# Performance work log

Measured on AMD Instinct MI355X. Metric: run time of the kernel, lower is better.

The kernel has to match this reference:

```python
import jax, jax.numpy as jnp
import numpy as np

N_USERS = 100000
N_ITEMS = 50000
N = N_USERS + N_ITEMS          # total graph nodes (users + items)
E = 128                        # emb_size
NNZ = 4_800_000                # edges per sparse adjacency (avg degree 32)
B = 4096                       # lookup batch
NL = 3                         # n_layers


def setup_inputs() -> dict:
    key = jax.random.key(0)
    ks = jax.random.split(key, 12)
    user_emb = jax.random.normal(ks[0], (N_USERS, E), jnp.float32) * 0.05
    item_emb = jax.random.normal(ks[1], (N_ITEMS, E), jnp.float32) * 0.05
    # COO edge lists for low-pass and high-pass normalized adjacencies.
    adj_row = jax.random.randint(ks[2], (NNZ,), 0, N)
    adj_col = jax.random.randint(ks[3], (NNZ,), 0, N)
    adj_val = jax.random.uniform(ks[4], (NNZ,), jnp.float32) / 32.0  # ~normalized weights
    hp_row = jax.random.randint(ks[5], (NNZ,), 0, N)
    hp_col = jax.random.randint(ks[6], (NNZ,), 0, N)
    hp_val = jax.random.uniform(ks[7], (NNZ,), jnp.float32) / 32.0
    # per-layer Linear(2E -> E): weight stored as [in, out] so y = x @ W + b
    W = jax.random.normal(ks[8], (NL, 2 * E, E), jnp.float32) * (1.0 / np.sqrt(2 * E))
    b = jnp.zeros((NL, E), jnp.float32)
    users = jax.random.randint(ks[9], (B,), 0, N_USERS)
    items = jax.random.randint(ks[10], (B,), 0, N_ITEMS)
    return dict(user_emb=user_emb, item_emb=item_emb, adj_val=adj_val, hp_val=hp_val,
                W=W, b=b, adj_row=adj_row, adj_col=adj_col,
                hp_row=hp_row, hp_col=hp_col, users=users, items=items)


def spmm(row, col, val, x):
    # sparse [N,N] @ dense [N,E] via gather + segment-sum
    return jax.ops.segment_sum(val[:, None] * x[col], row, num_segments=N)


def reference(user_emb, item_emb, adj_val, hp_val, W, b,
              adj_row, adj_col, hp_row, hp_col, users, items):
    ego = jnp.concatenate([user_emb, item_emb], axis=0)  # [N, E]
    pos = ego
    dis = ego
    for k in range(NL):
        pos = spmm(adj_row, adj_col, adj_val, pos)       # low-pass propagation
        dis = spmm(hp_row, hp_col, hp_val, dis)          # high-pass propagation
        ego = jnp.concatenate([pos, dis], axis=1) @ W[k] + b[k]  # [N, E]
        pos = ego
        dis = ego
    user_out = ego[users]                 # ego[:N_USERS][users]
    item_out = ego[N_USERS + items]       # ego[N_USERS:][items]
    return (user_out, item_out)
```

## Files before the change

kernel.cpp:

```cpp
#include <hip/hip_runtime.h>

#define N_USERS 100000
#define N_ITEMS 50000
#define NTOT    150000
#define E       128
#define NNZ     4800000
#define BATCH   4096
#define TILE    16
#define BSH     10
#define BROWS   1024
#define NBK     147
#define SLOT    16

typedef int v4i __attribute__((ext_vector_type(4)));

__device__ __forceinline__ int   ldnt_i(const int* p)   { return __builtin_nontemporal_load(p); }
__device__ __forceinline__ float ldnt_f(const float* p) { return __builtin_nontemporal_load(p); }
__device__ __forceinline__ v4i   ld_v4(const void* p)   { return *(const v4i*)p; }

__global__ __launch_bounds__(1024) void bucket_count(const int* __restrict__ rowA,
                                                     const int* __restrict__ rowH,
                                                     int* __restrict__ cntA,
                                                     int* __restrict__ cntH) {
    __shared__ int c[2 * NBK];
    for (int i = threadIdx.x; i < 2 * NBK; i += 1024) c[i] = 0;
    __syncthreads();
    int i = blockIdx.x * 1024 + threadIdx.x;
    const int stride = gridDim.x * 1024;
    for (; i < NNZ; i += stride) {
        atomicAdd(&c[ldnt_i(rowA + i) >> BSH], 1);
        atomicAdd(&c[NBK + (ldnt_i(rowH + i) >> BSH)], 1);
    }
    __syncthreads();
    for (int j = threadIdx.x; j < 2 * NBK; j += 1024) {
        const int v = c[j];
        if (v) atomicAdd(j < NBK ? (cntA + j) : (cntH + (j - NBK)), v);
    }
}

__global__ __launch_bounds__(64) void bucket_scan(const int* __restrict__ cntA,
                                                  const int* __restrict__ cntH,
                                                  int* __restrict__ baseA, int* __restrict__ baseH,
                                                  int* __restrict__ gcurA, int* __restrict__ gcurH) {
    const int t = threadIdx.x;
    if (t == 0) {
        int run = 0;
        for (int j = 0; j < NBK; ++j) { baseA[j] = run; gcurA[j] = run; run += cntA[j]; }
        baseA[NBK] = run;
    } else if (t == 1) {
        int run = 0;
        for (int j = 0; j < NBK; ++j) { baseH[j] = run; gcurH[j] = run; run += cntH[j]; }
        baseH[NBK] = run;
    }
}

__global__ __launch_bounds__(1024) void wc_scatter(const int* __restrict__ rowA, const int* __restrict__ colA,
                                                   const float* __restrict__ valA,
                                                   const int* __restrict__ rowH, const int* __restrict__ colH,
                                                   const float* __restrict__ valH,
                                                   int* __restrict__ gcurA, int* __restrict__ gcurH,
                                                   int2* __restrict__ stA, int2* __restrict__ stH) {
    __shared__ int  lcnt[2 * NBK];
    __shared__ int2 lent[2 * NBK * SLOT];
    for (int i = threadIdx.x; i < 2 * NBK; i += 1024) lcnt[i] = 0;
    __syncthreads();
    const int stride = gridDim.x * 1024;
    const int rounds = (NNZ + stride - 1) / stride;
    for (int rd = 0; rd < rounds; ++rd) {
        const int i = rd * stride + blockIdx.x * 1024 + threadIdx.x;
        if (i < NNZ) {
            {
                const int r = ldnt_i(rowA + i), cc = ldnt_i(colA + i);
                const float v = ldnt_f(valA + i);
                const int b = r >> BSH;
                const int2 pk = make_int2(((r & (BROWS - 1)) << 18) | cc, __float_as_int(v));
                const int n = atomicAdd(&lcnt[b], 1);
                if (n < SLOT) lent[b * SLOT + n] = pk;
                else          stA[atomicAdd(&gcurA[b], 1)] = pk;
            }
            {
                const int r = ldnt_i(rowH + i), cc = ldnt_i(colH + i);
                const float v = ldnt_f(valH + i);
                const int b = r >> BSH;
                const int gb = NBK + b;
                const int2 pk = make_int2(((r & (BROWS - 1)) << 18) | cc, __float_as_int(v));
                const int n = atomicAdd(&lcnt[gb], 1);
                if (n < SLOT) lent[gb * SLOT + n] = pk;
                else          stH[atomicAdd(&gcurH[b], 1)] = pk;
            }
        }
        __syncthreads();
        const int thresh = (rd == rounds - 1) ? 1 : 8;
        for (int gb = threadIdx.x; gb < 2 * NBK; gb += 1024) {
            int n = lcnt[gb]; if (n > SLOT) n = SLOT;
            if (n >= thresh) {
                int*  gc = (gb < NBK) ? &gcurA[gb] : &gcurH[gb - NBK];
                int2* st = (gb < NBK) ? stA : stH;
                const int p = atomicAdd(gc, n);
                for (int j = 0; j < n; ++j) st[p + j] = lent[gb * SLOT + j];
                lcnt[gb] = 0;
            }
        }
        __syncthreads();
    }
}

__global__ __launch_bounds__(1024) void bucket_csr(const int2* __restrict__ stA, const int2* __restrict__ stH,
                                                   const int* __restrict__ baseA, const int* __restrict__ baseH,
                                                   int* __restrict__ rpA, int* __restrict__ rpH,
                                                   int2* __restrict__ edA, int2* __restrict__ edH) {
    const int isH = blockIdx.x >= NBK;
    const int b   = isH ? blockIdx.x - NBK : blockIdx.x;
    const int2* st   = isH ? stH   : stA;
    const int*  base = isH ? baseH : baseA;
    int*  rp = isH ? rpH : rpA;
    int2* ed = isH ? edH : edA;
    const int s = base[b], e = base[b + 1];
    const int t = threadIdx.x, lane = t & 63, wv = t >> 6;
    __shared__ int cnt[BROWS];
    __shared__ int wsum[16], woff[16];
    cnt[t] = 0;
    __syncthreads();
    for (int i = s + t; i < e; i += 1024) atomicAdd(&cnt[st[i].x >> 18], 1);
    __syncthreads();
    const int v = cnt[t];
    int x = v;
    #pragma unroll
    for (int off = 1; off < 64; off <<= 1) {
        const int n = __shfl_up(x, off);
        if (lane >= off) x += n;
    }
    if (lane == 63) wsum[wv] = x;
    __syncthreads();
    if (t == 0) { int acc = 0; for (int w = 0; w < 16; ++w) { woff[w] = acc; acc += wsum[w]; } }
    __syncthreads();
    const int excl = woff[wv] + (x - v);
    const int rglob = (b << BSH) + t;
    if (rglob < NTOT) rp[rglob] = s + excl;
    __syncthreads();
    cnt[t] = excl;
    __syncthreads();
    for (int i = s + t; i < e; i += 1024) {
        const int2 pk = st[i];
        const int rl = pk.x >> 18;
        const int p = s + atomicAdd(&cnt[rl], 1);
        ed[p] = make_int2(pk.x & 0x3FFFF, pk.y);
    }
    if (t == 0 && b == 0) rp[NTOT] = NNZ;
}

__global__ __launch_bounds__(256) void copy_int(const int* __restrict__ src,
                                                int* __restrict__ dst, int n) {
    const int i = blockIdx.x * blockDim.x + threadIdx.x;
    if (i < n) dst[i] = src[i];
}

template<bool FIRST>
__device__ __forceinline__ const float4* rowbase(int c, const float* __restrict__ ue,
                                                 const float* __restrict__ ie,
                                                 const float* __restrict__ A) {
    if constexpr (FIRST)
        return (c < N_USERS) ? ((const float4*)ue + (size_t)c * (E / 4))
                             : ((const float4*)ie + (size_t)(c - N_USERS) * (E / 4));
    else
        return (const float4*)A + (size_t)c * (E / 4);
}

template<bool FIRST>
__device__ __forceinline__ void pairfma(v4i q, const float* __restrict__ ue,
                                        const float* __restrict__ ie,
                                        const float* __restrict__ A,
                                        int sub, int half, float4& acc) {
    const int   c = half ? q[2] : q[0];
    const float v = __int_as_float(half ? q[3] : q[1]);
    const float4 xv = rowbase<FIRST>(c, ue, ie, A)[sub];
    acc.x = fmaf(v, xv.x, acc.x);
    acc.y = fmaf(v, xv.y, acc.y);
    acc.z = fmaf(v, xv.z, acc.z);
    acc.w = fmaf(v, xv.w, acc.w);
}

template<bool FIRST>
__device__ __forceinline__ float4 row_accum(const int* __restrict__ rp,
                                            const int2* __restrict__ ed,
                                            const float* __restrict__ ue,
                                            const float* __restrict__ ie,
                                            const float* __restrict__ A,
                                            int r, int sub, int half) {
    const int s = rp[r];
    const int e = rp[r + 1];
    float4 accA = {0.f, 0.f, 0.f, 0.f};
    float4 accB = {0.f, 0.f, 0.f, 0.f};
    int i = s;
    if (i < e && (i & 1)) {
        const int2 t0 = ed[i];
        const float v = half ? 0.f : __int_as_float(t0.y);
        const float4 xv = rowbase<FIRST>(t0.x, ue, ie, A)[sub];
        accA.x = fmaf(v, xv.x, accA.x); accA.y = fmaf(v, xv.y, accA.y);
        accA.z = fmaf(v, xv.z, accA.z); accA.w = fmaf(v, xv.w, accA.w);
        ++i;
    }
    for (; i + 7 < e; i += 8) {
        const v4i q0 = ld_v4(ed + i);
        const v4i q1 = ld_v4(ed + i + 2);
        const v4i q2 = ld_v4(ed + i + 4);
        const v4i q3 = ld_v4(ed + i + 6);
        pairfma<FIRST>(q0, ue, ie, A, sub, half, accA);
        pairfma<FIRST>(q1, ue, ie, A, sub, half, accB);
        pairfma<FIRST>(q2, ue, ie, A, sub, half, accA);
        pairfma<FIRST>(q3, ue, ie, A, sub, half, accB);
    }
    for (; i + 1 < e; i += 2) {
        const v4i q = ld_v4(ed + i);
        pairfma<FIRST>(q, ue, ie, A, sub, half, accA);
    }
    if (i < e) {
        const int2 t0 = ed[i];
        const float v = half ? 0.f : __int_as_float(t0.y);
        const float4 xv = rowbase<FIRST>(t0.x, ue, ie, A)[sub];
        accA.x = fmaf(v, xv.x, accA.x); accA.y = fmaf(v, xv.y, accA.y);
        accA.z = fmaf(v, xv.z, accA.z); accA.w = fmaf(v, xv.w, accA.w);
    }
    return make_float4(accA.x + accB.x, accA.y + accB.y,
                       accA.z + accB.z, accA.w + accB.w);
}

template<bool FIRST, bool FINAL>
__global__ __launch_bounds__(256) void fused_layer(
    const float* __restrict__ A,
    const float* __restrict__ ue, const float* __restrict__ ie,
    const int* __restrict__ rpA, const int2* __restrict__ edA,
    const int* __restrict__ rpH, const int2* __restrict__ edH,
    const float* __restrict__ Wk, const float* __restrict__ bk,
    const int* __restrict__ users, const int* __restrict__ items,
    float* __restrict__ out) {
    __shared__ float sP[TILE][E];
    __shared__ float sD[TILE][E];
    const int t    = threadIdx.x;
    const int lane = t & 63;
    const int sub  = lane & 31;
    const int half = lane >> 5;
    const int wv   = t >> 6;
    const int r0   = blockIdx.x * TILE;

    for (int rl = wv * 4; rl < wv * 4 + 4; ++rl) {
        const int slot = r0 + rl;
        int r = slot;
        if constexpr (FINAL)
            r = (slot < BATCH) ? users[slot] : (N_USERS + items[slot - BATCH]);
        const float4 ap = row_accum<FIRST>(rpA, edA, ue, ie, A, r, sub, half);
        const float4 ad = row_accum<FIRST>(rpH, edH, ue, ie, A, r, sub, half);
        float4 send = half ? ap : ad;
        float4 recv;
        recv.x = __shfl_xor(send.x, 32);
        recv.y = __shfl_xor(send.y, 32);
        recv.z = __shfl_xor(send.z, 32);
        recv.w = __shfl_xor(send.w, 32);
        if (!half) {
            ((float4*)&sP[rl][0])[sub] = make_float4(ap.x + recv.x, ap.y + recv.y,
                                                     ap.z + recv.z, ap.w + recv.w);
        } else {
            ((float4*)&sD[rl][0])[sub] = make_float4(ad.x + recv.x, ad.y + recv.y,
                                                     ad.z + recv.z, ad.w + recv.w);
        }
    }
    __syncthreads();

    const int j = t & (E - 1);
    const int h = t >> 7;
    float acc[8];
    const float bj = bk[j];
    #pragma unroll
    for (int rr = 0; rr < 8; ++rr) acc[rr] = bj;

    #pragma unroll 4
    for (int i = 0; i < E; ++i) {
        const float w = Wk[(size_t)i * E + j];
        #pragma unroll
        for (int rr = 0; rr < 8; ++rr) acc[rr] = fmaf(sP[h * 8 + rr][i], w, acc[rr]);
    }
    #pragma unroll 4
    for (int i = 0; i < E; ++i) {
        const float w = Wk[(size_t)(E + i) * E + j];
        #pragma unroll
        for (int rr = 0; rr < 8; ++rr) acc[rr] = fmaf(sD[h * 8 + rr][i], w, acc[rr]);
    }

    #pragma unroll
    for (int rr = 0; rr < 8; ++rr) {
        float* p = &out[(size_t)(r0 + h * 8 + rr) * E + j];
        if constexpr (FIRST) __builtin_nontemporal_store(acc[rr], p);
        else                 *p = acc[rr];
    }
}

extern "C" void kernel_launch(void* const* d_in, const int* in_sizes, int n_in,
                              void* d_out, int out_size, void* d_ws, size_t ws_size,
                              hipStream_t stream) {
    const float* user_emb = (const float*)d_in[0];
    const float* item_emb = (const float*)d_in[1];
    const float* adj_val  = (const float*)d_in[2];
    const float* hp_val   = (const float*)d_in[3];
    const float* W        = (const float*)d_in[4];
    const float* bias     = (const float*)d_in[5];
    const int*   adj_row  = (const int*)d_in[6];
    const int*   adj_col  = (const int*)d_in[7];
    const int*   hp_row   = (const int*)d_in[8];
    const int*   hp_col   = (const int*)d_in[9];
    const int*   users    = (const int*)d_in[10];
    const int*   items    = (const int*)d_in[11];
    float* out = (float*)d_out;

    float* buf0 = (float*)d_ws;
    float* buf1 = buf0 + (size_t)NTOT * E;
    int2*  edA  = (int2*)(buf1 + (size_t)NTOT * E);
    int2*  edH  = edA + NNZ;
    int2*  stA  = (int2*)buf0;
    int2*  stH  = stA + NNZ;

    int* rpA   = (int*)d_out;
    int* rpH   = rpA + (NTOT + 1);
    int* cntA  = rpH + (NTOT + 1);
    int* cntH  = cntA + NBK;
    int* baseA = cntH + NBK;
    int* baseH = baseA + (NBK + 1);
    int* gcurA = baseH + (NBK + 1);
    int* gcurH = gcurA + NBK;
    int* rpA2 = (int*)buf1;
    int* rpH2 = rpA2 + (NTOT + 1);

    hipMemsetAsync(cntA, 0, (size_t)2 * NBK * sizeof(int), stream);
    bucket_count<<<256, 1024, 0, stream>>>(adj_row, hp_row, cntA, cntH);
    bucket_scan<<<1, 64, 0, stream>>>(cntA, cntH, baseA, baseH, gcurA, gcurH);
    wc_scatter<<<256, 1024, 0, stream>>>(adj_row, adj_col, adj_val,
                                         hp_row, hp_col, hp_val,
                                         gcurA, gcurH, stA, stH);
    bucket_csr<<<2 * NBK, 1024, 0, stream>>>(stA, stH, baseA, baseH, rpA, rpH, edA, edH);

    const int gridF = NTOT / TILE;
    const int gridL = (2 * BATCH) / TILE;
    fused_layer<true, false><<<gridF, 256, 0, stream>>>(
        nullptr, user_emb, item_emb, rpA, edA, rpH, edH,
        W, bias, nullptr, nullptr, buf1);
    fused_layer<false, false><<<gridF, 256, 0, stream>>>(
        buf1, nullptr, nullptr, rpA, edA, rpH, edH,
        W + (size_t)2 * E * E, bias + E, nullptr, nullptr, buf0);
    copy_int<<<(2 * (NTOT + 1) + 255) / 256, 256, 0, stream>>>(rpA, rpA2, 2 * (NTOT + 1));
    fused_layer<false, true><<<gridL, 256, 0, stream>>>(
        buf0, nullptr, nullptr, rpA2, edA, rpH2, edH,
        W + (size_t)4 * E * E, bias + 2 * E, users, items, out);
}
```

Before: 1.815 ms.

## Group rows by four and sort edges by column segment for gather locality

Replaces per-row CSR with groups of four rows whose edges are sorted by column segment, using byte-offset metadata per segment. Each wavefront walks the segments for its four rows together, so gathered source rows from nearby columns share cache across all waves in flight, and each lane loads a float2 slice. Layer kernels are split into five sub-launches over row ranges, and the final layer scans whole groups while filtering by row tag. This adds metadata cost, branchy per-edge accumulator selection, and a wasted scan of non-matching edges in the final layer.

```diff
diff --git a/kernel.cpp b/kernel.cpp
--- a/kernel.cpp
+++ b/kernel.cpp
@@ -11,12 +11,15 @@
 #define BROWS   1024
 #define NBK     147
 #define SLOT    16
-
-typedef int v4i __attribute__((ext_vector_type(4)));
+#define NSEG    37
+#define SEGSH   12
+#define NGRP    37500
+#define GPB     256
+#define NKEY    (GPB * NSEG)
+#define SUBL    1875
 
 __device__ __forceinline__ int   ldnt_i(const int* p)   { return __builtin_nontemporal_load(p); }
 __device__ __forceinline__ float ldnt_f(const float* p) { return __builtin_nontemporal_load(p); }
-__device__ __forceinline__ v4i   ld_v4(const void* p)   { return *(const v4i*)p; }
 
 __global__ __launch_bounds__(1024) void bucket_count(const int* __restrict__ rowA,
                                                      const int* __restrict__ rowH,
@@ -105,48 +108,71 @@
     }
 }
 
-__global__ __launch_bounds__(1024) void bucket_csr(const int2* __restrict__ stA, const int2* __restrict__ stH,
-                                                   const int* __restrict__ baseA, const int* __restrict__ baseH,
-                                                   int* __restrict__ rpA, int* __restrict__ rpH,
-                                                   int2* __restrict__ edA, int2* __restrict__ edH) {
+__global__ __launch_bounds__(1024) void bucket_csr_seg(
+    const int2* __restrict__ stA, const int2* __restrict__ stH,
+    const int* __restrict__ baseA, const int* __restrict__ baseH,
+    int* __restrict__ gbaseA, int* __restrict__ gbaseH,
+    unsigned char* __restrict__ relA, unsigned char* __restrict__ relH,
+    int2* __restrict__ edA, int2* __restrict__ edH) {
     const int isH = blockIdx.x >= NBK;
     const int b   = isH ? blockIdx.x - NBK : blockIdx.x;
     const int2* st   = isH ? stH   : stA;
     const int*  base = isH ? baseH : baseA;
-    int*  rp = isH ? rpH : rpA;
+    int*  gbase = isH ? gbaseH : gbaseA;
+    unsigned char* rel = isH ? relH : relA;
     int2* ed = isH ? edH : edA;
     const int s = base[b], e = base[b + 1];
     const int t = threadIdx.x, lane = t & 63, wv = t >> 6;
-    __shared__ int cnt[BROWS];
+    __shared__ int cnt[NKEY + 1];
     __shared__ int wsum[16], woff[16];
-    cnt[t] = 0;
-    __syncthreads();
-    for (int i = s + t; i < e; i += 1024) atomicAdd(&cnt[st[i].x >> 18], 1);
-    __syncthreads();
-    const int v = cnt[t];
-    int x = v;
-    #pragma unroll
-    for (int off = 1; off < 64; off <<= 1) {
-        const int n = __shfl_up(x, off);
-        if (lane >= off) x += n;
-    }
-    if (lane == 63) wsum[wv] = x;
-    __syncthreads();
-    if (t == 0) { int acc = 0; for (int w = 0; w < 16; ++w) { woff[w] = acc; acc += wsum[w]; } }
-    __syncthreads();
-    const int excl = woff[wv] + (x - v);
-    const int rglob = (b << BSH) + t;
-    if (rglob < NTOT) rp[rglob] = s + excl;
-    __syncthreads();
-    cnt[t] = excl;
+    __shared__ int carry, chtot;
+    for (int i = t; i <= NKEY; i += 1024) cnt[i] = 0;
+    if (t == 0) carry = 0;
+    __syncthreads();
+    for (int i = s + t; i < e; i += 1024) {
+        const int pk = st[i].x;
+        const int key = (pk >> 20) * NSEG + ((pk & 0x3FFFF) >> SEGSH);
+        atomicAdd(&cnt[key], 1);
+    }
+    __syncthreads();
+    for (int b2 = 0; b2 < NKEY; b2 += 1024) {
+        const int idx = b2 + t;
+        const int v = (idx < NKEY) ? cnt[idx] : 0;
+        int x = v;
+        #pragma unroll
+        for (int off = 1; off < 64; off <<= 1) {
+            const int n = __shfl_up(x, off);
+            if (lane >= off) x += n;
+        }
+        if (lane == 63) wsum[wv] = x;
+        __syncthreads();
+        if (t == 0) { int a = 0; for (int w = 0; w < 16; ++w) { woff[w] = a; a += wsum[w]; } chtot = a; }
+        __syncthreads();
+        if (idx < NKEY) cnt[idx] = carry + woff[wv] + (x - v);
+        __syncthreads();
+        if (t == 0) carry += chtot;
+        __syncthreads();
+    }
+    if (t == 0) cnt[NKEY] = e - s;
+    __syncthreads();
+    if (t < GPB) {
+        const int g = b * GPB + t;
+        if (g < NGRP) {
+            const int g0 = cnt[t * NSEG];
+            gbase[g] = s + g0;
+            const size_t rb = (size_t)g * 38;
+            for (int sg = 0; sg < NSEG; ++sg)
+                rel[rb + sg] = (unsigned char)(cnt[t * NSEG + sg] - g0);
+            rel[rb + NSEG] = (unsigned char)(cnt[(t + 1) * NSEG] - g0);
+        }
+    }
     __syncthreads();
     for (int i = s + t; i < e; i += 1024) {
         const int2 pk = st[i];
-        const int rl = pk.x >> 18;
-        const int p = s + atomicAdd(&cnt[rl], 1);
-        ed[p] = make_int2(pk.x & 0x3FFFF, pk.y);
-    }
-    if (t == 0 && b == 0) rp[NTOT] = NNZ;
+        const int key = (pk.x >> 20) * NSEG + ((pk.x & 0x3FFFF) >> SEGSH);
+        const int p = s + atomicAdd(&cnt[key], 1);
+        ed[p] = make_int2((((pk.x >> 18) & 3) << 18) | (pk.x & 0x3FFFF), pk.y);
+    }
 }
 
 __global__ __launch_bounds__(256) void copy_int(const int* __restrict__ src,
@@ -156,114 +182,94 @@
 }
 
 template<bool FIRST>
-__device__ __forceinline__ const float4* rowbase(int c, const float* __restrict__ ue,
-                                                 const float* __restrict__ ie,
-                                                 const float* __restrict__ A) {
+__device__ __forceinline__ float2 ldrow(int c, const float* __restrict__ ue,
+                                        const float* __restrict__ ie,
+                                        const float* __restrict__ A, int lane) {
+    const float* base;
     if constexpr (FIRST)
-        return (c < N_USERS) ? ((const float4*)ue + (size_t)c * (E / 4))
-                             : ((const float4*)ie + (size_t)(c - N_USERS) * (E / 4));
+        base = (c < N_USERS) ? (ue + (size_t)c * E) : (ie + (size_t)(c - N_USERS) * E);
     else
-        return (const float4*)A + (size_t)c * (E / 4);
-}
+        base = A + (size_t)c * E;
+    return ((const float2*)base)[lane];
+}
+
+#define FMA4(rl, v, xv, a0, a1, a2, a3)                                      \
+    do {                                                                      \
+        if      (rl == 0) { a0.x = fmaf(v, xv.x, a0.x); a0.y = fmaf(v, xv.y, a0.y); } \
+        else if (rl == 1) { a1.x = fmaf(v, xv.x, a1.x); a1.y = fmaf(v, xv.y, a1.y); } \
+        else if (rl == 2) { a2.x = fmaf(v, xv.x, a2.x); a2.y = fmaf(v, xv.y, a2.y); } \
+        else              { a3.x = fmaf(v, xv.x, a3.x); a3.y = fmaf(v, xv.y, a3.y); } \
+    } while (0)
 
 template<bool FIRST>
-__device__ __forceinline__ void pairfma(v4i q, const float* __restrict__ ue,
-                                        const float* __restrict__ ie,
-                                        const float* __restrict__ A,
-                                        int sub, int half, float4& acc) {
-    const int   c = half ? q[2] : q[0];
-    const float v = __int_as_float(half ? q[3] : q[1]);
-    const float4 xv = rowbase<FIRST>(c, ue, ie, A)[sub];
-    acc.x = fmaf(v, xv.x, acc.x);
-    acc.y = fmaf(v, xv.y, acc.y);
-    acc.z = fmaf(v, xv.z, acc.z);
-    acc.w = fmaf(v, xv.w, acc.w);
-}
-
-template<bool FIRST>
-__device__ __forceinline__ float4 row_accum(const int* __restrict__ rp,
-                                            const int2* __restrict__ ed,
-                                            const float* __restrict__ ue,
-                                            const float* __restrict__ ie,
-                                            const float* __restrict__ A,
-                                            int r, int sub, int half) {
-    const int s = rp[r];
-    const int e = rp[r + 1];
-    float4 accA = {0.f, 0.f, 0.f, 0.f};
-    float4 accB = {0.f, 0.f, 0.f, 0.f};
-    int i = s;
-    if (i < e && (i & 1)) {
-        const int2 t0 = ed[i];
-        const float v = half ? 0.f : __int_as_float(t0.y);
-        const float4 xv = rowbase<FIRST>(t0.x, ue, ie, A)[sub];
-        accA.x = fmaf(v, xv.x, accA.x); accA.y = fmaf(v, xv.y, accA.y);
-        accA.z = fmaf(v, xv.z, accA.z); accA.w = fmaf(v, xv.w, accA.w);
-        ++i;
-    }
-    for (; i + 7 < e; i += 8) {
-        const v4i q0 = ld_v4(ed + i);
-        const v4i q1 = ld_v4(ed + i + 2);
-        const v4i q2 = ld_v4(ed + i + 4);
-        const v4i q3 = ld_v4(ed + i + 6);
-        pairfma<FIRST>(q0, ue, ie, A, sub, half, accA);
-        pairfma<FIRST>(q1, ue, ie, A, sub, half, accB);
-        pairfma<FIRST>(q2, ue, ie, A, sub, half, accA);
-        pairfma<FIRST>(q3, ue, ie, A, sub, half, accB);
-    }
-    for (; i + 1 < e; i += 2) {
-        const v4i q = ld_v4(ed + i);
-        pairfma<FIRST>(q, ue, ie, A, sub, half, accA);
-    }
-    if (i < e) {
-        const int2 t0 = ed[i];
-        const float v = half ? 0.f : __int_as_float(t0.y);
-        const float4 xv = rowbase<FIRST>(t0.x, ue, ie, A)[sub];
-        accA.x = fmaf(v, xv.x, accA.x); accA.y = fmaf(v, xv.y, accA.y);
-        accA.z = fmaf(v, xv.z, accA.z); accA.w = fmaf(v, xv.w, accA.w);
-    }
-    return make_float4(accA.x + accB.x, accA.y + accB.y,
-                       accA.z + accB.z, accA.w + accB.w);
-}
-
-template<bool FIRST, bool FINAL>
-__global__ __launch_bounds__(256) void fused_layer(
+__global__ __launch_bounds__(256, 8) void fused_seg(
     const float* __restrict__ A,
     const float* __restrict__ ue, const float* __restrict__ ie,
-    const int* __restrict__ rpA, const int2* __restrict__ edA,
-    const int* __restrict__ rpH, const int2* __restrict__ edH,
+    const int* __restrict__ gbaseA, const unsigned char* __restrict__ relA,
+    const int2* __restrict__ edA,
+    const int* __restrict__ gbaseH, const unsigned char* __restrict__ relH,
+    const int2* __restrict__ edH,
     const float* __restrict__ Wk, const float* __restrict__ bk,
-    const int* __restrict__ users, const int* __restrict__ items,
-    float* __restrict__ out) {
+    int row0, float* __restrict__ out) {
     __shared__ float sP[TILE][E];
     __shared__ float sD[TILE][E];
-    const int t    = threadIdx.x;
-    const int lane = t & 63;
-    const int sub  = lane & 31;
-    const int half = lane >> 5;
-    const int wv   = t >> 6;
-    const int r0   = blockIdx.x * TILE;
-
-    for (int rl = wv * 4; rl < wv * 4 + 4; ++rl) {
-        const int slot = r0 + rl;
-        int r = slot;
-        if constexpr (FINAL)
-            r = (slot < BATCH) ? users[slot] : (N_USERS + items[slot - BATCH]);
-        const float4 ap = row_accum<FIRST>(rpA, edA, ue, ie, A, r, sub, half);
-        const float4 ad = row_accum<FIRST>(rpH, edH, ue, ie, A, r, sub, half);
-        float4 send = half ? ap : ad;
-        float4 recv;
-        recv.x = __shfl_xor(send.x, 32);
-        recv.y = __shfl_xor(send.y, 32);
-        recv.z = __shfl_xor(send.z, 32);
-        recv.w = __shfl_xor(send.w, 32);
-        if (!half) {
-            ((float4*)&sP[rl][0])[sub] = make_float4(ap.x + recv.x, ap.y + recv.y,
-                                                     ap.z + recv.z, ap.w + recv.w);
-        } else {
-            ((float4*)&sD[rl][0])[sub] = make_float4(ad.x + recv.x, ad.y + recv.y,
-                                                     ad.z + recv.z, ad.w + recv.w);
-        }
-    }
+    const int t = threadIdx.x, lane = t & 63, wv = t >> 6;
+    const int g = (row0 >> 2) + blockIdx.x * 4 + wv;
+    const int gbA = gbaseA[g], gbH = gbaseH[g];
+    const size_t rb = (size_t)g * 38;
+    float2 p0{0,0}, p1{0,0}, p2{0,0}, p3{0,0};
+    float2 d0{0,0}, d1{0,0}, d2{0,0}, d3{0,0};
+
+    for (int seg = 0; seg < NSEG; ++seg) {
+        {
+            int i = gbA + relA[rb + seg];
+            const int e = gbA + relA[rb + seg + 1];
+            for (; i + 1 < e; i += 2) {
+                const int2 e0 = edA[i], e1 = edA[i + 1];
+                const float2 x0 = ldrow<FIRST>(e0.x & 0x3FFFF, ue, ie, A, lane);
+                const float2 x1 = ldrow<FIRST>(e1.x & 0x3FFFF, ue, ie, A, lane);
+                const float v0 = __int_as_float(e0.y), v1 = __int_as_float(e1.y);
+                const int r0_ = e0.x >> 18, r1_ = e1.x >> 18;
+                FMA4(r0_, v0, x0, p0, p1, p2, p3);
+                FMA4(r1_, v1, x1, p0, p1, p2, p3);
+            }
+            if (i < e) {
+                const int2 e0 = edA[i];
+                const float2 x0 = ldrow<FIRST>(e0.x & 0x3FFFF, ue, ie, A, lane);
+                const float v0 = __int_as_float(e0.y);
+                const int r0_ = e0.x >> 18;
+                FMA4(r0_, v0, x0, p0, p1, p2, p3);
+            }
+        }
+        {
+            int i = gbH + relH[rb + seg];
+            const int e = gbH + relH[rb + seg + 1];
+            for (; i + 1 < e; i += 2) {
+                const int2 e0 = edH[i], e1 = edH[i + 1];
+                const float2 x0 = ldrow<FIRST>(e0.x & 0x3FFFF, ue, ie, A, lane);
+                const float2 x1 = ldrow<FIRST>(e1.x & 0x3FFFF, ue, ie, A, lane);
+                const float v0 = __int_as_float(e0.y), v1 = __int_as_float(e1.y);
+                const int r0_ = e0.x >> 18, r1_ = e1.x >> 18;
+                FMA4(r0_, v0, x0, d0, d1, d2, d3);
+                FMA4(r1_, v1, x1, d0, d1, d2, d3);
+            }
+            if (i < e) {
+                const int2 e0 = edH[i];
+                const float2 x0 = ldrow<FIRST>(e0.x & 0x3FFFF, ue, ie, A, lane);
+                const float v0 = __int_as_float(e0.y);
+                const int r0_ = e0.x >> 18;
+                FMA4(r0_, v0, x0, d0, d1, d2, d3);
+            }
+        }
+    }
+    ((float2*)&sP[wv * 4 + 0][0])[lane] = p0;
+    ((float2*)&sP[wv * 4 + 1][0])[lane] = p1;
+    ((float2*)&sP[wv * 4 + 2][0])[lane] = p2;
+    ((float2*)&sP[wv * 4 + 3][0])[lane] = p3;
+    ((float2*)&sD[wv * 4 + 0][0])[lane] = d0;
+    ((float2*)&sD[wv * 4 + 1][0])[lane] = d1;
+    ((float2*)&sD[wv * 4 + 2][0])[lane] = d2;
+    ((float2*)&sD[wv * 4 + 3][0])[lane] = d3;
     __syncthreads();
 
     const int j = t & (E - 1);
@@ -272,7 +278,6 @@
     const float bj = bk[j];
     #pragma unroll
     for (int rr = 0; rr < 8; ++rr) acc[rr] = bj;
-
     #pragma unroll 4
     for (int i = 0; i < E; ++i) {
         const float w = Wk[(size_t)i * E + j];
@@ -285,13 +290,81 @@
         #pragma unroll
         for (int rr = 0; rr < 8; ++rr) acc[rr] = fmaf(sD[h * 8 + rr][i], w, acc[rr]);
     }
-
     #pragma unroll
-    for (int rr = 0; rr < 8; ++rr) {
-        float* p = &out[(size_t)(r0 + h * 8 + rr) * E + j];
-        if constexpr (FIRST) __builtin_nontemporal_store(acc[rr], p);
-        else                 *p = acc[rr];
-    }
+    for (int rr = 0; rr < 8; ++rr)
+        out[(size_t)(row0 + blockIdx.x * TILE + h * 8 + rr) * E + j] = acc[rr];
+}
+
+__global__ __launch_bounds__(256) void fused_final(
+    const float* __restrict__ A,
+    const int* __restrict__ gbaseA, const unsigned char* __restrict__ relA,
+    const int2* __restrict__ edA,
+    const int* __restrict__ gbaseH, const unsigned char* __restrict__ relH,
+    const int2* __restrict__ edH,
+    const float* __restrict__ Wk, const float* __restrict__ bk,
+    const int* __restrict__ users, const int* __restrict__ items,
+    float* __restrict__ out) {
+    __shared__ float sP[TILE][E];
+    __shared__ float sD[TILE][E];
+    const int t = threadIdx.x, lane = t & 63, wv = t >> 6;
+
+    #pragma unroll
+    for (int q = 0; q < 4; ++q) {
+        const int slot = blockIdx.x * TILE + wv * 4 + q;
+        const int r = (slot < BATCH) ? users[slot] : (N_USERS + items[slot - BATCH]);
+        const int g = r >> 2, rl = r & 3;
+        float2 ap{0,0};
+        {
+            int i = gbaseA[g];
+            const int e = i + relA[(size_t)g * 38 + NSEG];
+            for (; i < e; ++i) {
+                const int2 ee = edA[i];
+                if ((ee.x >> 18) == rl) {
+                    const float2 xv = ((const float2*)(A + (size_t)(ee.x & 0x3FFFF) * E))[lane];
+                    const float v = __int_as_float(ee.y);
+                    ap.x = fmaf(v, xv.x, ap.x); ap.y = fmaf(v, xv.y, ap.y);
+                }
+            }
+        }
+        ((float2*)&sP[wv * 4 + q][0])[lane] = ap;
+        float2 ad{0,0};
+        {
+            int i = gbaseH[g];
+            const int e = i + relH[(size_t)g * 38 + NSEG];
+            for (; i < e; ++i) {
+                const int2 ee = edH[i];
+                if ((ee.x >> 18) == rl) {
+                    const float2 xv = ((const float2*)(A + (size_t)(ee.x & 0x3FFFF) * E))[lane];
+                    const float v = __int_as_float(ee.y);
+                    ad.x = fmaf(v, xv.x, ad.x); ad.y = fmaf(v, xv.y, ad.y);
+                }
+            }
+        }
+        ((float2*)&sD[wv * 4 + q][0])[lane] = ad;
+    }
+    __syncthreads();
+
+    const int j = t & (E - 1);
+    const int h = t >> 7;
+    float acc[8];
+    const float bj = bk[j];
+    #pragma unroll
+    for (int rr = 0; rr < 8; ++rr) acc[rr] = bj;
+    #pragma unroll 4
+    for (int i = 0; i < E; ++i) {
+        const float w = Wk[(size_t)i * E + j];
+        #pragma unroll
+        for (int rr = 0; rr < 8; ++rr) acc[rr] = fmaf(sP[h * 8 + rr][i], w, acc[rr]);
+    }
+    #pragma unroll 4
+    for (int i = 0; i < E; ++i) {
+        const float w = Wk[(size_t)(E + i) * E + j];
+        #pragma unroll
+        for (int rr = 0; rr < 8; ++rr) acc[rr] = fmaf(sD[h * 8 + rr][i], w, acc[rr]);
+    }
+    #pragma unroll
+    for (int rr = 0; rr < 8; ++rr)
+        out[(size_t)(blockIdx.x * TILE + h * 8 + rr) * E + j] = acc[rr];
 }
 
 extern "C" void kernel_launch(void* const* d_in, const int* in_sizes, int n_in,
@@ -318,16 +391,22 @@
     int2*  stA  = (int2*)buf0;
     int2*  stH  = stA + NNZ;
 
-    int* rpA   = (int*)d_out;
-    int* rpH   = rpA + (NTOT + 1);
-    int* cntA  = rpH + (NTOT + 1);
+    int* gbA_d = (int*)d_out;
+    int* gbH_d = gbA_d + NGRP;
+    unsigned char* relA_d = (unsigned char*)(gbH_d + NGRP);
+    unsigned char* relH_d = relA_d + (size_t)NGRP * 38;
+    int* cntA  = (int*)(relH_d + (size_t)NGRP * 38);
     int* cntH  = cntA + NBK;
     int* baseA = cntH + NBK;
     int* baseH = baseA + (NBK + 1);
     int* gcurA = baseH + (NBK + 1);
     int* gcurH = gcurA + NBK;
-    int* rpA2 = (int*)buf1;
-    int* rpH2 = rpA2 + (NTOT + 1);
+    const int META_INTS = (2 * NGRP * 4 + 2 * NGRP * 38) / 4;
+
+    int* gbA_f = (int*)buf1;
+    int* gbH_f = gbA_f + NGRP;
+    unsigned char* relA_f = (unsigned char*)(gbH_f + NGRP);
+    unsigned char* relH_f = relA_f + (size_t)NGRP * 38;
 
     hipMemsetAsync(cntA, 0, (size_t)2 * NBK * sizeof(int), stream);
     bucket_count<<<256, 1024, 0, stream>>>(adj_row, hp_row, cntA, cntH);
@@ -335,18 +414,20 @@
     wc_scatter<<<256, 1024, 0, stream>>>(adj_row, adj_col, adj_val,
                                          hp_row, hp_col, hp_val,
                                          gcurA, gcurH, stA, stH);
-    bucket_csr<<<2 * NBK, 1024, 0, stream>>>(stA, stH, baseA, baseH, rpA, rpH, edA, edH);
-
-    const int gridF = NTOT / TILE;
-    const int gridL = (2 * BATCH) / TILE;
-    fused_layer<true, false><<<gridF, 256, 0, stream>>>(
-        nullptr, user_emb, item_emb, rpA, edA, rpH, edH,
-        W, bias, nullptr, nullptr, buf1);
-    fused_layer<false, false><<<gridF, 256, 0, stream>>>(
-        buf1, nullptr, nullptr, rpA, edA, rpH, edH,
-        W + (size_t)2 * E * E, bias + E, nullptr, nullptr, buf0);
-    copy_int<<<(2 * (NTOT + 1) + 255) / 256, 256, 0, stream>>>(rpA, rpA2, 2 * (NTOT + 1));
-    fused_layer<false, true><<<gridL, 256, 0, stream>>>(
-        buf0, nullptr, nullptr, rpA2, edA, rpH2, edH,
+    bucket_csr_seg<<<2 * NBK, 1024, 0, stream>>>(stA, stH, baseA, baseH,
+                                                 gbA_d, gbH_d, relA_d, relH_d, edA, edH);
+
+    for (int s5 = 0; s5 < 5; ++s5)
+        fused_seg<true><<<SUBL, 256, 0, stream>>>(
+            nullptr, user_emb, item_emb, gbA_d, relA_d, edA, gbH_d, relH_d, edH,
+            W, bias, s5 * SUBL * TILE, buf1);
+    for (int s5 = 0; s5 < 5; ++s5)
+        fused_seg<false><<<SUBL, 256, 0, stream>>>(
+            buf1, nullptr, nullptr, gbA_d, relA_d, edA, gbH_d, relH_d, edH,
+            W + (size_t)2 * E * E, bias + E, s5 * SUBL * TILE, buf0);
+
+    copy_int<<<(META_INTS + 255) / 256, 256, 0, stream>>>(gbA_d, gbA_f, META_INTS);
+    fused_final<<<(2 * BATCH) / TILE, 256, 0, stream>>>(
+        buf0, gbA_f, relA_f, edA, gbH_f, relH_f, edH,
         W + (size_t)4 * E * E, bias + 2 * E, users, items, out);
 }
```

Measured after the change: 2.778 ms. 1.53x slower.

## Split full-layer SpMM into two column-half passes to shrink gather working set

Applied to the files above, without the earlier changes.

Each of the first two layers is now split into two kernels. The first gathers only columns 0-63 of neighbour rows and stages the partial sums in the output buffer. The second gathers columns 64-127, reloads the staged first half and does the dense Linear. Halving the gathered row footprint per pass is meant to raise L2/MALL hit rates on random neighbour rows, at the cost of an extra CSR traversal, extra launches and a round trip of the intermediate through global memory. The bucket_count and wc_scatter grids are also doubled.

```diff
diff --git a/kernel.cpp b/kernel.cpp
--- a/kernel.cpp
+++ b/kernel.cpp
@@ -156,48 +156,40 @@
 }
 
 template<bool FIRST>
-__device__ __forceinline__ const float4* rowbase(int c, const float* __restrict__ ue,
-                                                 const float* __restrict__ ie,
-                                                 const float* __restrict__ A) {
+__device__ __forceinline__ const float* rowb(int c, const float* __restrict__ ue,
+                                             const float* __restrict__ ie,
+                                             const float* __restrict__ A) {
     if constexpr (FIRST)
-        return (c < N_USERS) ? ((const float4*)ue + (size_t)c * (E / 4))
-                             : ((const float4*)ie + (size_t)(c - N_USERS) * (E / 4));
+        return (c < N_USERS) ? (ue + (size_t)c * E) : (ie + (size_t)(c - N_USERS) * E);
     else
-        return (const float4*)A + (size_t)c * (E / 4);
-}
-
-template<bool FIRST>
-__device__ __forceinline__ void pairfma(v4i q, const float* __restrict__ ue,
+        return A + (size_t)c * E;
+}
+
+template<bool FIRST, int HALF>
+__device__ __forceinline__ void pf_half(v4i q, const float* __restrict__ ue,
                                         const float* __restrict__ ie,
                                         const float* __restrict__ A,
-                                        int sub, int half, float4& acc) {
+                                        int sub, int half, float2& acc) {
     const int   c = half ? q[2] : q[0];
     const float v = __int_as_float(half ? q[3] : q[1]);
-    const float4 xv = rowbase<FIRST>(c, ue, ie, A)[sub];
+    const float2 xv = ((const float2*)(rowb<FIRST>(c, ue, ie, A) + HALF * 64))[sub];
     acc.x = fmaf(v, xv.x, acc.x);
     acc.y = fmaf(v, xv.y, acc.y);
-    acc.z = fmaf(v, xv.z, acc.z);
-    acc.w = fmaf(v, xv.w, acc.w);
-}
-
-template<bool FIRST>
-__device__ __forceinline__ float4 row_accum(const int* __restrict__ rp,
-                                            const int2* __restrict__ ed,
-                                            const float* __restrict__ ue,
-                                            const float* __restrict__ ie,
-                                            const float* __restrict__ A,
-                                            int r, int sub, int half) {
-    const int s = rp[r];
-    const int e = rp[r + 1];
-    float4 accA = {0.f, 0.f, 0.f, 0.f};
-    float4 accB = {0.f, 0.f, 0.f, 0.f};
+}
+
+template<bool FIRST, int HALF>
+__device__ __forceinline__ float2 accum_half(int s, int e, const int2* __restrict__ ed,
+                                             const float* __restrict__ ue,
+                                             const float* __restrict__ ie,
+                                             const float* __restrict__ A,
+                                             int sub, int half) {
+    float2 a{0.f, 0.f}, b{0.f, 0.f};
     int i = s;
     if (i < e && (i & 1)) {
         const int2 t0 = ed[i];
         const float v = half ? 0.f : __int_as_float(t0.y);
-        const float4 xv = rowbase<FIRST>(t0.x, ue, ie, A)[sub];
-        accA.x = fmaf(v, xv.x, accA.x); accA.y = fmaf(v, xv.y, accA.y);
-        accA.z = fmaf(v, xv.z, accA.z); accA.w = fmaf(v, xv.w, accA.w);
+        const float2 xv = ((const float2*)(rowb<FIRST>(t0.x, ue, ie, A) + HALF * 64))[sub];
+        a.x = fmaf(v, xv.x, a.x); a.y = fmaf(v, xv.y, a.y);
         ++i;
     }
     for (; i + 7 < e; i += 8) {
@@ -205,30 +197,163 @@
         const v4i q1 = ld_v4(ed + i + 2);
         const v4i q2 = ld_v4(ed + i + 4);
         const v4i q3 = ld_v4(ed + i + 6);
-        pairfma<FIRST>(q0, ue, ie, A, sub, half, accA);
-        pairfma<FIRST>(q1, ue, ie, A, sub, half, accB);
-        pairfma<FIRST>(q2, ue, ie, A, sub, half, accA);
-        pairfma<FIRST>(q3, ue, ie, A, sub, half, accB);
+        pf_half<FIRST, HALF>(q0, ue, ie, A, sub, half, a);
+        pf_half<FIRST, HALF>(q1, ue, ie, A, sub, half, b);
+        pf_half<FIRST, HALF>(q2, ue, ie, A, sub, half, a);
+        pf_half<FIRST, HALF>(q3, ue, ie, A, sub, half, b);
     }
     for (; i + 1 < e; i += 2) {
         const v4i q = ld_v4(ed + i);
-        pairfma<FIRST>(q, ue, ie, A, sub, half, accA);
+        pf_half<FIRST, HALF>(q, ue, ie, A, sub, half, a);
     }
     if (i < e) {
         const int2 t0 = ed[i];
         const float v = half ? 0.f : __int_as_float(t0.y);
-        const float4 xv = rowbase<FIRST>(t0.x, ue, ie, A)[sub];
-        accA.x = fmaf(v, xv.x, accA.x); accA.y = fmaf(v, xv.y, accA.y);
-        accA.z = fmaf(v, xv.z, accA.z); accA.w = fmaf(v, xv.w, accA.w);
-    }
-    return make_float4(accA.x + accB.x, accA.y + accB.y,
-                       accA.z + accB.z, accA.w + accB.w);
-}
-
-template<bool FIRST, bool FINAL>
-__global__ __launch_bounds__(256) void fused_layer(
+        const float2 xv = ((const float2*)(rowb<FIRST>(t0.x, ue, ie, A) + HALF * 64))[sub];
+        a.x = fmaf(v, xv.x, a.x); a.y = fmaf(v, xv.y, a.y);
+    }
+    return make_float2(a.x + b.x, a.y + b.y);
+}
+
+template<bool FIRST>
+__global__ __launch_bounds__(256) void fused_passA(
     const float* __restrict__ A,
     const float* __restrict__ ue, const float* __restrict__ ie,
+    const int* __restrict__ rpA, const int2* __restrict__ edA,
+    const int* __restrict__ rpH, const int2* __restrict__ edH,
+    float* __restrict__ outb) {
+    const int t = threadIdx.x, lane = t & 63, sub = lane & 31, half = lane >> 5, wv = t >> 6;
+    const int r0 = blockIdx.x * TILE;
+    #pragma unroll
+    for (int rl = 0; rl < 4; ++rl) {
+        const int r = r0 + wv * 4 + rl;
+        const float2 ap = accum_half<FIRST, 0>(rpA[r], rpA[r + 1], edA, ue, ie, A, sub, half);
+        const float2 ad = accum_half<FIRST, 0>(rpH[r], rpH[r + 1], edH, ue, ie, A, sub, half);
+        float2 send = half ? ap : ad;
+        float2 recv;
+        recv.x = __shfl_xor(send.x, 32);
+        recv.y = __shfl_xor(send.y, 32);
+        if (!half) {
+            const float2 f{ap.x + recv.x, ap.y + recv.y};
+            ((float2*)(outb + (size_t)r * E))[sub] = f;
+        } else {
+            const float2 f{ad.x + recv.x, ad.y + recv.y};
+            ((float2*)(outb + (size_t)r * E + 64))[sub] = f;
+        }
+    }
+}
+
+template<bool FIRST>
+__global__ __launch_bounds__(256) void fused_passB(
+    const float* __restrict__ A,
+    const float* __restrict__ ue, const float* __restrict__ ie,
+    const int* __restrict__ rpA, const int2* __restrict__ edA,
+    const int* __restrict__ rpH, const int2* __restrict__ edH,
+    const float* __restrict__ Wk, const float* __restrict__ bk,
+    float* __restrict__ outb) {
+    __shared__ float sP[TILE][E];
+    __shared__ float sD[TILE][E];
+    const int t = threadIdx.x, lane = t & 63, sub = lane & 31, half = lane >> 5, wv = t >> 6;
+    const int r0 = blockIdx.x * TILE;
+    #pragma unroll
+    for (int rl = 0; rl < 4; ++rl) {
+        const int r = r0 + wv * 4 + rl;
+        const float2 ap = accum_half<FIRST, 1>(rpA[r], rpA[r + 1], edA, ue, ie, A, sub, half);
+        const float2 ad = accum_half<FIRST, 1>(rpH[r], rpH[r + 1], edH, ue, ie, A, sub, half);
+        float2 send = half ? ap : ad;
+        float2 recv;
+        recv.x = __shfl_xor(send.x, 32);
+        recv.y = __shfl_xor(send.y, 32);
+        if (!half) {
+            const float2 f{ap.x + recv.x, ap.y + recv.y};
+            ((float2*)&sP[wv * 4 + rl][64])[sub] = f;
+        } else {
+            const float2 f{ad.x + recv.x, ad.y + recv.y};
+            ((float2*)&sD[wv * 4 + rl][64])[sub] = f;
+        }
+    }
+    {
+        const int row = t >> 4;
+        const int q   = t & 15;
+        const float4 vp = *(const float4*)(outb + (size_t)(r0 + row) * E + q * 4);
+        const float4 vd = *(const float4*)(outb + (size_t)(r0 + row) * E + 64 + q * 4);
+        *(float4*)&sP[row][q * 4] = vp;
+        *(float4*)&sD[row][q * 4] = vd;
+    }
+    __syncthreads();
+
+    const int j = t & (E - 1);
+    const int h = t >> 7;
+    float acc[8];
+    const float bj = bk[j];
+    #pragma unroll
+    for (int rr = 0; rr < 8; ++rr) acc[rr] = bj;
+    #pragma unroll 4
+    for (int i = 0; i < E; ++i) {
+        const float w = Wk[(size_t)i * E + j];
+        #pragma unroll
+        for (int rr = 0; rr < 8; ++rr) acc[rr] = fmaf(sP[h * 8 + rr][i], w, acc[rr]);
+    }
+    #pragma unroll 4
+    for (int i = 0; i < E; ++i) {
+        const float w = Wk[(size_t)(E + i) * E + j];
+        #pragma unroll
+        for (int rr = 0; rr < 8; ++rr) acc[rr] = fmaf(sD[h * 8 + rr][i], w, acc[rr]);
+    }
+    #pragma unroll
+    for (int rr = 0; rr < 8; ++rr)
+        outb[(size_t)(r0 + h * 8 + rr) * E + j] = acc[rr];
+}
+
+__device__ __forceinline__ void pf_full(v4i q, const float* __restrict__ A,
+                                        int sub, int half, float4& acc) {
+    const int   c = half ? q[2] : q[0];
+    const float v = __int_as_float(half ? q[3] : q[1]);
+    const float4 xv = ((const float4*)(A + (size_t)c * E))[sub];
+    acc.x = fmaf(v, xv.x, acc.x);
+    acc.y = fmaf(v, xv.y, acc.y);
+    acc.z = fmaf(v, xv.z, acc.z);
+    acc.w = fmaf(v, xv.w, acc.w);
+}
+
+__device__ __forceinline__ float4 accum_full(int s, int e, const int2* __restrict__ ed,
+                                             const float* __restrict__ A, int sub, int half) {
+    float4 a{0.f,0.f,0.f,0.f}, b{0.f,0.f,0.f,0.f};
+    int i = s;
+    if (i < e && (i & 1)) {
+        const int2 t0 = ed[i];
+        const float v = half ? 0.f : __int_as_float(t0.y);
+        const float4 xv = ((const float4*)(A + (size_t)t0.x * E))[sub];
+        a.x = fmaf(v, xv.x, a.x); a.y = fmaf(v, xv.y, a.y);
+        a.z = fmaf(v, xv.z, a.z); a.w = fmaf(v, xv.w, a.w);
+        ++i;
+    }
+    for (; i + 7 < e; i += 8) {
+        const v4i q0 = ld_v4(ed + i);
+        const v4i q1 = ld_v4(ed + i + 2);
+        const v4i q2 = ld_v4(ed + i + 4);
+        const v4i q3 = ld_v4(ed + i + 6);
+        pf_full(q0, A, sub, half, a);
+        pf_full(q1, A, sub, half, b);
+        pf_full(q2, A, sub, half, a);
+        pf_full(q3, A, sub, half, b);
+    }
+    for (; i + 1 < e; i += 2) {
+        const v4i q = ld_v4(ed + i);
+        pf_full(q, A, sub, half, a);
+    }
+    if (i < e) {
+        const int2 t0 = ed[i];
+        const float v = half ? 0.f : __int_as_float(t0.y);
+        const float4 xv = ((const float4*)(A + (size_t)t0.x * E))[sub];
+        a.x = fmaf(v, xv.x, a.x); a.y = fmaf(v, xv.y, a.y);
+        a.z = fmaf(v, xv.z, a.z); a.w = fmaf(v, xv.w, a.w);
+    }
+    return make_float4(a.x + b.x, a.y + b.y, a.z + b.z, a.w + b.w);
+}
+
+__global__ __launch_bounds__(256) void fused_final(
+    const float* __restrict__ A,
     const int* __restrict__ rpA, const int2* __restrict__ edA,
     const int* __restrict__ rpH, const int2* __restrict__ edH,
     const float* __restrict__ Wk, const float* __restrict__ bk,
@@ -236,20 +361,14 @@
     float* __restrict__ out) {
     __shared__ float sP[TILE][E];
     __shared__ float sD[TILE][E];
-    const int t    = threadIdx.x;
-    const int lane = t & 63;
-    const int sub  = lane & 31;
-    const int half = lane >> 5;
-    const int wv   = t >> 6;
-    const int r0   = blockIdx.x * TILE;
-
-    for (int rl = wv * 4; rl < wv * 4 + 4; ++rl) {
-        const int slot = r0 + rl;
-        int r = slot;
-        if constexpr (FINAL)
-            r = (slot < BATCH) ? users[slot] : (N_USERS + items[slot - BATCH]);
-        const float4 ap = row_accum<FIRST>(rpA, edA, ue, ie, A, r, sub, half);
-        const float4 ad = row_accum<FIRST>(rpH, edH, ue, ie, A, r, sub, half);
+    const int t = threadIdx.x, lane = t & 63, sub = lane & 31, half = lane >> 5, wv = t >> 6;
+
+    #pragma unroll
+    for (int rl = 0; rl < 4; ++rl) {
+        const int slot = blockIdx.x * TILE + wv * 4 + rl;
+        const int r = (slot < BATCH) ? users[slot] : (N_USERS + items[slot - BATCH]);
+        const float4 ap = accum_full(rpA[r], rpA[r + 1], edA, A, sub, half);
+        const float4 ad = accum_full(rpH[r], rpH[r + 1], edH, A, sub, half);
         float4 send = half ? ap : ad;
         float4 recv;
         recv.x = __shfl_xor(send.x, 32);
@@ -257,11 +376,11 @@
         recv.z = __shfl_xor(send.z, 32);
         recv.w = __shfl_xor(send.w, 32);
         if (!half) {
-            ((float4*)&sP[rl][0])[sub] = make_float4(ap.x + recv.x, ap.y + recv.y,
-                                                     ap.z + recv.z, ap.w + recv.w);
+            ((float4*)&sP[wv * 4 + rl][0])[sub] = make_float4(ap.x + recv.x, ap.y + recv.y,
+                                                              ap.z + recv.z, ap.w + recv.w);
         } else {
-            ((float4*)&sD[rl][0])[sub] = make_float4(ad.x + recv.x, ad.y + recv.y,
-                                                     ad.z + recv.z, ad.w + recv.w);
+            ((float4*)&sD[wv * 4 + rl][0])[sub] = make_float4(ad.x + recv.x, ad.y + recv.y,
+                                                              ad.z + recv.z, ad.w + recv.w);
         }
     }
     __syncthreads();
@@ -272,7 +391,6 @@
     const float bj = bk[j];
     #pragma unroll
     for (int rr = 0; rr < 8; ++rr) acc[rr] = bj;
-
     #pragma unroll 4
     for (int i = 0; i < E; ++i) {
         const float w = Wk[(size_t)i * E + j];
@@ -285,13 +403,9 @@
         #pragma unroll
         for (int rr = 0; rr < 8; ++rr) acc[rr] = fmaf(sD[h * 8 + rr][i], w, acc[rr]);
     }
-
-    #pragma unroll
-    for (int rr = 0; rr < 8; ++rr) {
-        float* p = &out[(size_t)(r0 + h * 8 + rr) * E + j];
-        if constexpr (FIRST) __builtin_nontemporal_store(acc[rr], p);
-        else                 *p = acc[rr];
-    }
+    #pragma unroll
+    for (int rr = 0; rr < 8; ++rr)
+        out[(size_t)(blockIdx.x * TILE + h * 8 + rr) * E + j] = acc[rr];
 }
 
 extern "C" void kernel_launch(void* const* d_in, const int* in_sizes, int n_in,
@@ -326,27 +440,33 @@
     int* baseH = baseA + (NBK + 1);
     int* gcurA = baseH + (NBK + 1);
     int* gcurH = gcurA + NBK;
+
     int* rpA2 = (int*)buf1;
     int* rpH2 = rpA2 + (NTOT + 1);
 
     hipMemsetAsync(cntA, 0, (size_t)2 * NBK * sizeof(int), stream);
-    bucket_count<<<256, 1024, 0, stream>>>(adj_row, hp_row, cntA, cntH);
+    bucket_count<<<512, 1024, 0, stream>>>(adj_row, hp_row, cntA, cntH);
     bucket_scan<<<1, 64, 0, stream>>>(cntA, cntH, baseA, baseH, gcurA, gcurH);
-    wc_scatter<<<256, 1024, 0, stream>>>(adj_row, adj_col, adj_val,
+    wc_scatter<<<512, 1024, 0, stream>>>(adj_row, adj_col, adj_val,
                                          hp_row, hp_col, hp_val,
                                          gcurA, gcurH, stA, stH);
     bucket_csr<<<2 * NBK, 1024, 0, stream>>>(stA, stH, baseA, baseH, rpA, rpH, edA, edH);
 
     const int gridF = NTOT / TILE;
     const int gridL = (2 * BATCH) / TILE;
-    fused_layer<true, false><<<gridF, 256, 0, stream>>>(
-        nullptr, user_emb, item_emb, rpA, edA, rpH, edH,
-        W, bias, nullptr, nullptr, buf1);
-    fused_layer<false, false><<<gridF, 256, 0, stream>>>(
+
+    fused_passA<true><<<gridF, 256, 0, stream>>>(
+        nullptr, user_emb, item_emb, rpA, edA, rpH, edH, buf1);
+    fused_passB<true><<<gridF, 256, 0, stream>>>(
+        nullptr, user_emb, item_emb, rpA, edA, rpH, edH, W, bias, buf1);
+    fused_passA<false><<<gridF, 256, 0, stream>>>(
+        buf1, nullptr, nullptr, rpA, edA, rpH, edH, buf0);
+    fused_passB<false><<<gridF, 256, 0, stream>>>(
         buf1, nullptr, nullptr, rpA, edA, rpH, edH,
-        W + (size_t)2 * E * E, bias + E, nullptr, nullptr, buf0);
+        W + (size_t)2 * E * E, bias + E, buf0);
+
     copy_int<<<(2 * (NTOT + 1) + 255) / 256, 256, 0, stream>>>(rpA, rpA2, 2 * (NTOT + 1));
-    fused_layer<false, true><<<gridL, 256, 0, stream>>>(
-        buf0, nullptr, nullptr, rpA2, edA, rpH2, edH,
+    fused_final<<<gridL, 256, 0, stream>>>(
+        buf0, rpA2, edA, rpH2, edH,
         W + (size_t)4 * E * E, bias + 2 * E, users, items, out);
 }
```

After: 2.050 ms. 13.0% more time.
